# Optimization experiments

Measured on AMD Instinct MI355X. Metric: run time of the kernel, lower is better.

## Reference

```python
import jax, jax.numpy as jnp
import numpy as np

B, N, C = 4, 2304, 256
H = 8                      # num_heads
D = C // H                 # head_dim = 32
SCALE = D ** -0.5
H_DS, W_DS = 48, 48
UP = 2                     # spatial_down_ratio
EPS = 1e-5


def setup_inputs() -> dict:
    key = jax.random.key(0)
    ks = jax.random.split(key, 16)
    g = lambda k, shape, s: (jax.random.normal(k, shape, dtype=jnp.float32) * s)
    return {
        "x1": g(ks[0], (B, N, C), 1.0),
        "x2": g(ks[1], (B, N, C), 1.0),
        # attention projections (torch Linear convention: [out, in], no bias)
        "q1_w": g(ks[2], (C, C), C ** -0.5),
        "kv1_w": g(ks[3], (2 * C, C), C ** -0.5),
        "q2_w": g(ks[4], (C, C), C ** -0.5),
        "kv2_w": g(ks[5], (2 * C, C), C ** -0.5),
        # per-head scalar biases
        "beta12": jnp.full((H,), 0.2, dtype=jnp.float32),
        "beta21": jnp.full((H,), 0.1, dtype=jnp.float32),
        # output projections
        "p1_w": g(ks[6], (C, C), (2.0 / C) ** 0.5),
        "p1_b": g(ks[7], (C,), 1e-2),
        "p2_w": g(ks[8], (C, C), (2.0 / C) ** 0.5),
        "p2_b": g(ks[9], (C,), 1e-2),
        # LayerNorm affine params
        "g1": jnp.ones((C,), dtype=jnp.float32),
        "b1": jnp.zeros((C,), dtype=jnp.float32),
        "g2": jnp.ones((C,), dtype=jnp.float32),
        "b2": jnp.zeros((C,), dtype=jnp.float32),
    }


def _heads(x):
    # [B,N,C] -> [B,H,N,D]
    return x.reshape(B, N, H, D).transpose(0, 2, 1, 3)


def _merge(x):
    # [B,H,N,D] -> [B,N,C]
    return x.transpose(0, 2, 1, 3).reshape(B, N, C)


def _cross_attn(q, k, v, beta):
    # scores: [B,H,N,N] with per-head scalar bias
    s = jnp.einsum("bhqd,bhkd->bhqk", q, k) * SCALE + beta[None, :, None, None]
    a = jax.nn.softmax(s, axis=-1)
    return jnp.einsum("bhqk,bhkd->bhqd", a, v)


def _layernorm(x, g, b):
    mu = jnp.mean(x, axis=-1, keepdims=True)
    var = jnp.var(x, axis=-1, keepdims=True)
    return (x - mu) * jax.lax.rsqrt(var + EPS) * g + b


def _forward(x1, x2, q1_w, kv1_w, q2_w, kv2_w, beta12, beta21,
             p1_w, p1_b, p2_w, p2_b, g1, b1, g2, b2):
    q1 = _heads(x1 @ q1_w.T)
    kv1 = x1 @ kv1_w.T          # [B,N,2C]
    k1, v1 = _heads(kv1[..., :C]), _heads(kv1[..., C:])
    q2 = _heads(x2 @ q2_w.T)
    kv2 = x2 @ kv2_w.T
    k2, v2 = _heads(kv2[..., :C]), _heads(kv2[..., C:])

    o1 = _merge(_cross_attn(q1, k2, v2, beta12))   # x1 attends to x2
    o2 = _merge(_cross_attn(q2, k1, v1, beta21))   # x2 attends to x1

    y1 = _layernorm(jax.nn.relu(o1 @ p1_w.T + p1_b), g1, b1)
    y2 = _layernorm(jax.nn.relu(o2 @ p2_w.T + p2_b), g2, b2)

    # [B,N,C] -> [B,C,H_ds,W_ds]
    y1 = y1.transpose(0, 2, 1).reshape(B, C, H_DS, W_DS)
    y2 = y2.transpose(0, 2, 1).reshape(B, C, H_DS, W_DS)

    # bilinear upsample x2, align_corners=False (half-pixel == jax.image default)
    out_shape = (B, C, H_DS * UP, W_DS * UP)
    y1 = jax.image.resize(y1, out_shape, method="bilinear")
    y2 = jax.image.resize(y2, out_shape, method="bilinear")
    return y1, y2


def reference(x1, x2, q1_w, kv1_w, q2_w, kv2_w, beta12, beta21,
              p1_w, p1_b, p2_w, p2_b, g1, b1, g2, b2):
    return _forward(x1, x2, q1_w, kv1_w, q2_w, kv2_w, beta12, beta21,
                    p1_w, p1_b, p2_w, p2_b, g1, b1, g2, b2)
```

## Files before the change

### kernel.cpp

```cpp
#include <hip/hip_runtime.h>
#include <math.h>


typedef __attribute__((ext_vector_type(8))) short short8;
typedef __attribute__((ext_vector_type(4))) float f32x4;
typedef __attribute__((ext_vector_type(16))) float f32x16;
typedef __attribute__((ext_vector_type(2))) unsigned uint32x2;

#define MFMA16(a, b, c) __builtin_amdgcn_mfma_f32_16x16x32_bf16((a), (b), (c), 0, 0, 0)
#define MFMA32(a, b, c) __builtin_amdgcn_mfma_f32_32x32x16_bf16((a), (b), (c), 0, 0, 0)

__device__ __forceinline__ float bf2f(ushort u) {
    union { unsigned u; float f; } x; x.u = ((unsigned)u) << 16; return x.f;
}
__device__ __forceinline__ ushort f2bf(float f) {
    union { float f; unsigned u; } x; x.f = f;
    unsigned u = x.u;
    return (ushort)((u + 0x7fffu + ((u >> 16) & 1u)) >> 16);
}
__device__ __forceinline__ unsigned cvt_pk_bf16(float a, float b) {
    unsigned r;
    asm("v_cvt_pk_bf16_f32 %0, %1, %2" : "=v"(r) : "v"(a), "v"(b));
    return r;
}
__device__ __forceinline__ float fast_ex2(float x) {
    float r;
    asm("v_exp_f32 %0, %1" : "=v"(r) : "v"(x));
    return r;
}
__device__ __forceinline__ void plswap(unsigned &a, unsigned &b) {
    uint32x2 r = __builtin_amdgcn_permlane32_swap(a, b, false, false);
    a = r[0]; b = r[1];
}

__global__ __launch_bounds__(256) void prep_kernel(
    const void* __restrict__ x1, const void* __restrict__ x2,
    ushort* __restrict__ xo1, ushort* __restrict__ xo2,
    const void* s0, const void* s1, const void* s2, const void* s3,
    const void* s4, const void* s5, const void* s6, const void* s7,
    const void* s8, const void* s9, const void* s10, const void* s11,
    ushort* __restrict__ dst)
{
    ushort u = ((const ushort*)x1)[(threadIdx.x & 63) * 2];
    int e = (u >> 7) & 0xFF;
    int outlier = (e < 100 || e > 135) ? 1 : 0;
    unsigned long long mk = __ballot(outlier);
    int flag = (__popcll(mk) >= 16) ? 1 : 0;

    int bid = blockIdx.x;
    if (bid < 2304) {
        int idx = bid * 256 + threadIdx.x;
        int which = idx >= 294912;
        int off = (which ? idx - 294912 : idx) * 8;
        const void* src = which ? x2 : x1;
        ushort* o = which ? xo2 : xo1;
        if (flag) {
            const float* p = (const float*)src + off;
            float4 a = *(const float4*)p;
            float4 c = *(const float4*)(p + 4);
            uint4 u4;
            u4.x = cvt_pk_bf16(a.x, a.y);
            u4.y = cvt_pk_bf16(a.z, a.w);
            u4.z = cvt_pk_bf16(c.x, c.y);
            u4.w = cvt_pk_bf16(c.z, c.w);
            *(uint4*)(o + off) = u4;
        } else {
            *(uint4*)(o + off) = *(const uint4*)((const ushort*)src + off);
        }
    } else {
        int idx = (bid - 2304) * 256 + threadIdx.x;
        if (idx >= 525824) return;
        const void* src; int off;
        if      (idx < 65536)  { src = s0;  off = idx; }
        else if (idx < 196608) { src = s1;  off = idx - 65536; }
        else if (idx < 262144) { src = s2;  off = idx - 196608; }
        else if (idx < 393216) { src = s3;  off = idx - 262144; }
        else if (idx < 458752) { src = s4;  off = idx - 393216; }
        else if (idx < 524288) { src = s5;  off = idx - 458752; }
        else if (idx < 524544) { src = s6;  off = idx - 524288; }
        else if (idx < 524800) { src = s7;  off = idx - 524544; }
        else if (idx < 525056) { src = s8;  off = idx - 524800; }
        else if (idx < 525312) { src = s9;  off = idx - 525056; }
        else if (idx < 525568) { src = s10; off = idx - 525312; }
        else                   { src = s11; off = idx - 525568; }
        ushort v = flag ? f2bf(((const float*)src)[off])
                        : ((const ushort*)src)[off];
        dst[idx] = v;
    }
}

__global__ __launch_bounds__(256) void gemm_bt(
    const void* __restrict__ Ain, const ushort* __restrict__ W,
    ushort* __restrict__ C, const ushort* __restrict__ bias,
    int M, int N, int K, int relu, const int* __restrict__ dflag, int a_ext,
    int mode, ushort* __restrict__ Kh, ushort* __restrict__ Vt,
    const ushort* __restrict__ W2, const ushort* __restrict__ bias2,
    ushort* __restrict__ Kh2, ushort* __restrict__ Vt2, int mhalf)
{
    __shared__ __align__(16) ushort As[128][40];
    __shared__ __align__(16) ushort Ws[128][40];

    const int m0 = blockIdx.x * 128;
    const int n0 = blockIdx.y * 128;
    const int tid = threadIdx.x;
    const int w = tid >> 6;
    const int wr = w >> 1, wc = w & 1;
    const int lane = tid & 63;
    const int lm = lane & 15;
    const int quad = lane >> 4;
    const int a32 = a_ext ? *dflag : 0;

    const int side = (mhalf && m0 >= mhalf) ? 1 : 0;
    const ushort* Wu = side ? W2 : W;
    const ushort* bu = side ? bias2 : bias;
    ushort* Khu = side ? Kh2 : Kh;
    ushort* Vtu = side ? Vt2 : Vt;

    const f32x4 Z4 = {0.f, 0.f, 0.f, 0.f};
    f32x4 acc[4][4];
    for (int i = 0; i < 4; i++)
        for (int j = 0; j < 4; j++) acc[i][j] = Z4;

    const ushort* A16 = (const ushort*)Ain;
    const float*  A32 = (const float*)Ain;
    const int row = tid >> 1, off16 = (tid & 1) * 16;

    for (int k0 = 0; k0 < K; k0 += 32) {
        __syncthreads();
        if (a32) {
            const float* p0 = A32 + (size_t)(m0 + row) * K + k0 + off16;
            float4 f0 = *(const float4*)p0;
            float4 f1 = *(const float4*)(p0 + 4);
            float4 f2 = *(const float4*)(p0 + 8);
            float4 f3 = *(const float4*)(p0 + 12);
            uint4 t0, t1;
            t0.x = cvt_pk_bf16(f0.x, f0.y);
            t0.y = cvt_pk_bf16(f0.z, f0.w);
            t0.z = cvt_pk_bf16(f1.x, f1.y);
            t0.w = cvt_pk_bf16(f1.z, f1.w);
            t1.x = cvt_pk_bf16(f2.x, f2.y);
            t1.y = cvt_pk_bf16(f2.z, f2.w);
            t1.z = cvt_pk_bf16(f3.x, f3.y);
            t1.w = cvt_pk_bf16(f3.z, f3.w);
            *(uint4*)&As[row][off16]     = t0;
            *(uint4*)&As[row][off16 + 8] = t1;
        } else {
            const ushort* p0 = A16 + (size_t)(m0 + row) * K + k0 + off16;
            *(uint4*)&As[row][off16]     = *(const uint4*)p0;
            *(uint4*)&As[row][off16 + 8] = *(const uint4*)(p0 + 8);
        }
        {
            const ushort* p0 = Wu + (size_t)(n0 + row) * K + k0 + off16;
            *(uint4*)&Ws[row][off16]     = *(const uint4*)p0;
            *(uint4*)&Ws[row][off16 + 8] = *(const uint4*)(p0 + 8);
        }
        __syncthreads();

        short8 af[4], wf[4];
        #pragma unroll
        for (int mt = 0; mt < 4; mt++)
            af[mt] = *(const short8*)&As[wr * 64 + mt * 16 + lm][quad * 8];
        #pragma unroll
        for (int nt = 0; nt < 4; nt++)
            wf[nt] = *(const short8*)&Ws[wc * 64 + nt * 16 + lm][quad * 8];
        #pragma unroll
        for (int mt = 0; mt < 4; mt++)
            #pragma unroll
            for (int nt = 0; nt < 4; nt++)
                acc[mt][nt] = MFMA16(af[mt], wf[nt], acc[mt][nt]);
    }

    if (mode == 1) {
        const float QSC = 0.17677669529663687f * 1.4426950408889634f;
        #pragma unroll
        for (int mt = 0; mt < 4; mt++) {
            const int grow = m0 + wr * 64 + mt * 16 + quad * 4;
            const int grel = grow - (side ? mhalf : 0);
            int bb = grel / 2304;
            int tok = grel - bb * 2304;
            #pragma unroll
            for (int nt = 0; nt < 4; nt++) {
                int col = n0 + wc * 64 + nt * 16 + lm;
                if (col < 256) {
                    for (int r = 0; r < 4; r++)
                        C[(size_t)(grow + r) * 256 + col] = f2bf(acc[mt][nt][r] * QSC);
                } else if (col < 512) {
                    int c2 = col - 256, hh = c2 >> 5, d = c2 & 31;
                    size_t kb = ((size_t)(bb * 8 + hh) * 72 + (tok >> 5)) * 1024
                              + (size_t)(d >> 4) * 512 + (size_t)(d & 15);
                    for (int r = 0; r < 4; r++)
                        Khu[kb + (size_t)((tok + r) & 31) * 16] = f2bf(acc[mt][nt][r]);
                } else {
                    int c2 = col - 512, hh = c2 >> 5, d = c2 & 31;
                    size_t vb = ((size_t)(bb * 8 + hh) * 144 + (tok >> 4)) * 512
                              + (size_t)d * 16 + (size_t)(tok & 15);
                    uint2 o;
                    o.x = cvt_pk_bf16(acc[mt][nt][0], acc[mt][nt][1]);
                    o.y = cvt_pk_bf16(acc[mt][nt][2], acc[mt][nt][3]);
                    *(uint2*)&Vtu[vb] = o;
                }
            }
        }
    } else {
        #pragma unroll
        for (int mt = 0; mt < 4; mt++) {
            const int grow = m0 + wr * 64 + mt * 16 + quad * 4;
            #pragma unroll
            for (int nt = 0; nt < 4; nt++) {
                int col = n0 + wc * 64 + nt * 16 + lm;
                float bv = bu ? bf2f(bu[col]) : 0.f;
                for (int r = 0; r < 4; r++) {
                    float v = acc[mt][nt][r] + bv;
                    if (relu) v = fmaxf(v, 0.f);
                    C[(size_t)(grow + r) * N + col] = f2bf(v);
                }
            }
        }
    }
}

__global__ __launch_bounds__(256) void attn_kernel(
    const ushort* __restrict__ Qa, const ushort* __restrict__ Kha,
    const ushort* __restrict__ Vta, ushort* __restrict__ Oa,
    const ushort* __restrict__ Qb, const ushort* __restrict__ Khb2,
    const ushort* __restrict__ Vtb2, ushort* __restrict__ Ob)
{
    __shared__ unsigned Lo[4][2][64][8];
    __shared__ float    Ll[4][2][64];

    const int sid = blockIdx.x;
    const int qb = blockIdx.y;
    const int side = sid >> 5;
    const int bh = sid & 31;
    const ushort* Q  = side ? Qb   : Qa;
    const ushort* Kh = side ? Khb2 : Kha;
    const ushort* Vt = side ? Vtb2 : Vta;
    ushort* O        = side ? Ob   : Oa;

    const int b = bh >> 3, h = bh & 7;
    const int tid = threadIdx.x;
    const int w = tid >> 6, lane = tid & 63;
    const int l31 = lane & 31, hl = lane >> 5;

    const int qrow0 = qb * 64 + l31;
    const int qrow1 = qrow0 + 32;
    const ushort* qp0 = Q + ((size_t)b * 2304 + qrow0) * 256 + h * 32 + hl * 8;
    const ushort* qp1 = Q + ((size_t)b * 2304 + qrow1) * 256 + h * 32 + hl * 8;
    const short8 qf0a = *(const short8*)qp0;
    const short8 qf1a = *(const short8*)(qp0 + 16);
    const short8 qf0b = *(const short8*)qp1;
    const short8 qf1b = *(const short8*)(qp1 + 16);

    f32x16 oa, ob;
    #pragma unroll
    for (int i = 0; i < 16; i++) { oa[i] = 0.f; ob[i] = 0.f; }
    const f32x16 Z16 = oa;
    float la = 0.f, lb = 0.f;

    const ushort* kp0 = Kh + (size_t)bh * 73728 + l31 * 16 + hl * 8;
    const ushort* vp0 = Vt + (size_t)bh * 73728 + l31 * 16 + hl * 8;

#define LOADT(kf0v, kf1v, vf0v, vf1v, t) { \
    const ushort* _kp = kp0 + (size_t)(t) * 1024; \
    kf0v = *(const short8*)_kp; \
    kf1v = *(const short8*)(_kp + 512); \
    const ushort* _vp = vp0 + (size_t)(t) * 1024; \
    vf0v = *(const short8*)_vp; \
    vf1v = *(const short8*)(_vp + 512); \
}
#define QSET(kf0v, kf1v, vf0v, vf1v, qf0v, qf1v, oacc, lacc) { \
    f32x16 s = MFMA32(kf0v, qf0v, Z16); \
    s = MFMA32(kf1v, qf1v, s); \
    float p[16]; \
    _Pragma("unroll") \
    for (int i = 0; i < 16; i++) p[i] = fast_ex2(s[i]); \
    lacc += (((p[0] + p[1]) + (p[2] + p[3])) + ((p[4] + p[5]) + (p[6] + p[7]))) \
          + (((p[8] + p[9]) + (p[10] + p[11])) + ((p[12] + p[13]) + (p[14] + p[15]))); \
    unsigned c0 = cvt_pk_bf16(p[0],  p[1]); \
    unsigned c1 = cvt_pk_bf16(p[2],  p[3]); \
    unsigned c2 = cvt_pk_bf16(p[4],  p[5]); \
    unsigned c3 = cvt_pk_bf16(p[6],  p[7]); \
    unsigned c4 = cvt_pk_bf16(p[8],  p[9]); \
    unsigned c5 = cvt_pk_bf16(p[10], p[11]); \
    unsigned c6 = cvt_pk_bf16(p[12], p[13]); \
    unsigned c7 = cvt_pk_bf16(p[14], p[15]); \
    plswap(c0, c2); plswap(c1, c3); plswap(c4, c6); plswap(c5, c7); \
    union { unsigned u[4]; short8 s8; } pA, pB; \
    pA.u[0] = c0; pA.u[1] = c1; pA.u[2] = c2; pA.u[3] = c3; \
    pB.u[0] = c4; pB.u[1] = c5; pB.u[2] = c6; pB.u[3] = c7; \
    oacc = MFMA32(vf0v, pA.s8, oacc); \
    oacc = MFMA32(vf1v, pB.s8, oacc); \
}
#define COMP(kf0v, kf1v, vf0v, vf1v) { \
    QSET(kf0v, kf1v, vf0v, vf1v, qf0a, qf1a, oa, la); \
    QSET(kf0v, kf1v, vf0v, vf1v, qf0b, qf1b, ob, lb); \
}

    short8 kA0, kA1, vA0, vA1;
    short8 kB0, kB1, vB0, vB1;

    const int t0 = w * 18;

    LOADT(kA0, kA1, vA0, vA1, t0);
    LOADT(kB0, kB1, vB0, vB1, t0 + 1);

    for (int i = 0; i < 9; i++) {
        COMP(kA0, kA1, vA0, vA1);
        { int ta = t0 + 2 * i + 2; ta = ta < 72 ? ta : 70;
          LOADT(kA0, kA1, vA0, vA1, ta); }
        COMP(kB0, kB1, vB0, vB1);
        { int tb = t0 + 2 * i + 3; tb = tb < 72 ? tb : 71;
          LOADT(kB0, kB1, vB0, vB1, tb); }
    }
#undef LOADT
#undef QSET
#undef COMP

    la += __shfl_xor(la, 32, 64);
    lb += __shfl_xor(lb, 32, 64);

    #pragma unroll
    for (int r = 0; r < 8; r++) {
        Lo[w][0][lane][r] = cvt_pk_bf16(oa[2 * r], oa[2 * r + 1]);
        Lo[w][1][lane][r] = cvt_pk_bf16(ob[2 * r], ob[2 * r + 1]);
    }
    Ll[w][0][lane] = la;
    Ll[w][1][lane] = lb;
    __syncthreads();

    if (w < 2) {
        float os[16];
        #pragma unroll
        for (int r = 0; r < 16; r++) os[r] = 0.f;
        float ls = 0.f;
        #pragma unroll
        for (int u = 0; u < 4; u++) {
            ls += Ll[u][w][lane];
            #pragma unroll
            for (int r = 0; r < 8; r++) {
                unsigned pv = Lo[u][w][lane][r];
                os[2 * r]     += bf2f((ushort)pv);
                os[2 * r + 1] += bf2f((ushort)(pv >> 16));
            }
        }
        float rl = 1.f / ls;
        const int qrow = (w == 0) ? qrow0 : qrow1;
        ushort* op = O + ((size_t)b * 2304 + qrow) * 256 + h * 32 + hl * 4;
        #pragma unroll
        for (int g = 0; g < 4; g++) {
            uint2 o;
            o.x = cvt_pk_bf16(os[4 * g] * rl, os[4 * g + 1] * rl);
            o.y = cvt_pk_bf16(os[4 * g + 2] * rl, os[4 * g + 3] * rl);
            *(uint2*)(op + 8 * g) = o;
        }
    }
}

__global__ __launch_bounds__(256) void projlnt_kernel(
    const ushort* __restrict__ O,
    const ushort* __restrict__ W1c, const ushort* __restrict__ b1v,
    const ushort* __restrict__ g1v, const ushort* __restrict__ t1v,
    const ushort* __restrict__ W2c, const ushort* __restrict__ b2v,
    const ushort* __restrict__ g2v, const ushort* __restrict__ t2v,
    ushort* __restrict__ Yt)
{
    __shared__ __align__(16) ushort As[64][40];
    __shared__ __align__(16) ushort Ws[256][40];
    __shared__ float Sred[4][64][2];

    const int m0 = blockIdx.x * 64;
    const int side = (m0 >= 9216) ? 1 : 0;
    const ushort* Wu = side ? W2c : W1c;
    const ushort* bu = side ? b2v : b1v;
    const ushort* gu = side ? g2v : g1v;
    const ushort* tu = side ? t2v : t1v;

    const int tid = threadIdx.x;
    const int w = tid >> 6, lane = tid & 63;
    const int lm = lane & 15, quad = lane >> 4;

    const f32x4 Z4 = {0.f, 0.f, 0.f, 0.f};
    f32x4 acc[4][4];
    for (int i = 0; i < 4; i++)
        for (int j = 0; j < 4; j++) acc[i][j] = Z4;

    const int arow = tid >> 2, aoff = (tid & 3) * 8;

    for (int k0 = 0; k0 < 256; k0 += 32) {
        __syncthreads();
        *(uint4*)&As[arow][aoff] =
            *(const uint4*)(O + (size_t)(m0 + arow) * 256 + k0 + aoff);
        const ushort* wp = Wu + (size_t)tid * 256 + k0;
        *(uint4*)&Ws[tid][0]  = *(const uint4*)(wp);
        *(uint4*)&Ws[tid][8]  = *(const uint4*)(wp + 8);
        *(uint4*)&Ws[tid][16] = *(const uint4*)(wp + 16);
        *(uint4*)&Ws[tid][24] = *(const uint4*)(wp + 24);
        __syncthreads();

        short8 af[4], wf[4];
        #pragma unroll
        for (int mt = 0; mt < 4; mt++)
            af[mt] = *(const short8*)&As[mt * 16 + lm][quad * 8];
        #pragma unroll
        for (int nt = 0; nt < 4; nt++)
            wf[nt] = *(const short8*)&Ws[w * 64 + nt * 16 + lm][quad * 8];
        #pragma unroll
        for (int mt = 0; mt < 4; mt++)
            #pragma unroll
            for (int nt = 0; nt < 4; nt++)
                acc[mt][nt] = MFMA16(af[mt], wf[nt], acc[mt][nt]);
    }

    #pragma unroll
    for (int nt = 0; nt < 4; nt++) {
        float bv = bf2f(bu[w * 64 + nt * 16 + lm]);
        #pragma unroll
        for (int mt = 0; mt < 4; mt++)
            #pragma unroll
            for (int r = 0; r < 4; r++)
                acc[mt][nt][r] = fmaxf(acc[mt][nt][r] + bv, 0.f);
    }

    float s[4][4], q[4][4];
    #pragma unroll
    for (int mt = 0; mt < 4; mt++)
        #pragma unroll
        for (int r = 0; r < 4; r++) {
            float a0 = acc[mt][0][r], a1 = acc[mt][1][r];
            float a2 = acc[mt][2][r], a3 = acc[mt][3][r];
            s[mt][r] = (a0 + a1) + (a2 + a3);
            q[mt][r] = (a0 * a0 + a1 * a1) + (a2 * a2 + a3 * a3);
        }
    #pragma unroll
    for (int off = 1; off < 16; off <<= 1)
        #pragma unroll
        for (int mt = 0; mt < 4; mt++)
            #pragma unroll
            for (int r = 0; r < 4; r++) {
                s[mt][r] += __shfl_xor(s[mt][r], off, 64);
                q[mt][r] += __shfl_xor(q[mt][r], off, 64);
            }
    if (lm == 0) {
        #pragma unroll
        for (int mt = 0; mt < 4; mt++)
            #pragma unroll
            for (int r = 0; r < 4; r++) {
                int rowl = mt * 16 + quad * 4 + r;
                Sred[w][rowl][0] = s[mt][r];
                Sred[w][rowl][1] = q[mt][r];
            }
    }
    __syncthreads();

    const int mrel = m0 - side * 9216;
    const int bb = mrel / 2304;
    const int tokb = mrel - bb * 2304;
    #pragma unroll
    for (int mt = 0; mt < 4; mt++) {
        float mu[4], rs[4];
        #pragma unroll
        for (int r = 0; r < 4; r++) {
            int rowl = mt * 16 + quad * 4 + r;
            float S = (Sred[0][rowl][0] + Sred[1][rowl][0])
                    + (Sred[2][rowl][0] + Sred[3][rowl][0]);
            float Qq = (Sred[0][rowl][1] + Sred[1][rowl][1])
                     + (Sred[2][rowl][1] + Sred[3][rowl][1]);
            float m = S * (1.f / 256.f);
            float var = Qq * (1.f / 256.f) - m * m;
            mu[r] = m;
            rs[r] = rsqrtf(var + 1e-5f);
        }
        #pragma unroll
        for (int nt = 0; nt < 4; nt++) {
            int col = w * 64 + nt * 16 + lm;
            float g = bf2f(gu[col]);
            float bt = bf2f(tu[col]);
            float y0 = (acc[mt][nt][0] - mu[0]) * rs[0] * g + bt;
            float y1 = (acc[mt][nt][1] - mu[1]) * rs[1] * g + bt;
            float y2 = (acc[mt][nt][2] - mu[2]) * rs[2] * g + bt;
            float y3 = (acc[mt][nt][3] - mu[3]) * rs[3] * g + bt;
            uint2 o;
            o.x = cvt_pk_bf16(y0, y1);
            o.y = cvt_pk_bf16(y2, y3);
            size_t base = ((size_t)((side * 4 + bb) * 256 + col)) * 2304
                        + tokb + mt * 16 + quad * 4;
            *(uint2*)(Yt + base) = o;
        }
    }
}

__global__ __launch_bounds__(256) void upsample_kernel(
    const ushort* __restrict__ Yt, float* __restrict__ out)
{
    int idx = blockIdx.x * 256 + threadIdx.x;
    int t  = idx % 24;
    int r_ = idx / 24;
    int oi = r_ % 96;
    int bc = r_ / 96;

    float fi = oi * 0.5f - 0.25f;
    int i0 = (int)floorf(fi);
    float wi = fi - (float)i0;
    int i1 = i0 + 1 < 47 ? i0 + 1 : 47;
    i0 = i0 > 0 ? i0 : 0;
    int j0 = 2 * t;
    int jm = j0 - 1 > 0 ? j0 - 1 : 0;
    int jp = j0 + 2 < 47 ? j0 + 2 : 47;

    const ushort* r0 = Yt + (size_t)bc * 2304 + i0 * 48;
    const ushort* r1 = Yt + (size_t)bc * 2304 + i1 * 48;
    float a0 = bf2f(r0[jm]), b0 = bf2f(r0[j0]), c0 = bf2f(r0[j0 + 1]), d0 = bf2f(r0[jp]);
    float a1 = bf2f(r1[jm]), b1 = bf2f(r1[j0]), c1 = bf2f(r1[j0 + 1]), d1 = bf2f(r1[jp]);
    float u = 1.f - wi;
    float ha = u * a0 + wi * a1;
    float hb = u * b0 + wi * b1;
    float hc = u * c0 + wi * c1;
    float hd = u * d0 + wi * d1;
    float4 o;
    o.x = 0.25f * ha + 0.75f * hb;
    o.y = 0.75f * hb + 0.25f * hc;
    o.z = 0.25f * hb + 0.75f * hc;
    o.w = 0.75f * hc + 0.25f * hd;
    *(float4*)(out + (size_t)bc * 9216 + oi * 96 + t * 4) = o;
}

extern "C" void kernel_launch(void* const* d_in, const int* in_sizes, int n_in,
                              void* d_out, int out_size, void* d_ws, size_t ws_size,
                              hipStream_t stream)
{
    (void)in_sizes; (void)n_in; (void)out_size; (void)ws_size;

    ushort* ws  = (ushort*)d_ws;
    ushort* Q1  = ws;
    ushort* Q2  = Q1  + 2359296;
    ushort* KV1 = Q2  + 2359296;
    ushort* KV2 = KV1 + 4718592;
    ushort* wc  = KV2 + 4718592;

    ushort* cqkv1w = wc;
    ushort* cqkv2w = wc + 196608;
    ushort* cp1w  = wc + 393216;
    ushort* cp2w  = wc + 458752;
    ushort* cp1b  = wc + 524288;
    ushort* cp2b  = wc + 524544;
    ushort* cg1   = wc + 524800;
    ushort* cb1   = wc + 525056;
    ushort* cg2   = wc + 525312;
    ushort* cb2   = wc + 525568;

    float*  outf = (float*)d_out;
    ushort* O1  = (ushort*)d_out;
    ushort* O2  = O1 + 2359296;
    ushort* Xb1 = O2 + 2359296;
    ushort* Xb2 = Xb1 + 2359296;
    ushort* Yt  = Q1;
    (void)Q2; (void)O2; (void)Xb2;

    dim3 blk(256);
    prep_kernel<<<dim3(4358), blk, 0, stream>>>(
        d_in[0], d_in[1], Xb1, Xb2,
        d_in[2], d_in[3], d_in[4], d_in[5], d_in[8], d_in[10],
        d_in[9], d_in[11], d_in[12], d_in[13], d_in[14], d_in[15],
        wc);

    gemm_bt<<<dim3(144, 6), blk, 0, stream>>>(Xb1, cqkv1w, Q1, nullptr,
        18432, 768, 256, 0, nullptr, 0, 1, KV1, KV1 + 2359296,
        cqkv2w, nullptr, KV2, KV2 + 2359296, 9216);

    attn_kernel<<<dim3(64, 36), blk, 0, stream>>>(
        Q1, KV2, KV2 + 2359296, O1,
        Q2, KV1, KV1 + 2359296, O2);

    projlnt_kernel<<<dim3(288), blk, 0, stream>>>(
        O1, cp1w, cp1b, cg1, cb1, cp2w, cp2b, cg2, cb2, Yt);

    upsample_kernel<<<dim3(18432), blk, 0, stream>>>(Yt, outf);
}
```

Measured before the change: 244.0 us.

## Halve attention query tile per block and spread final reduction across all waves

Each attention block now handles 32 query rows instead of 64, doubling the grid to 64x72 blocks. Each wave runs one QK/PV chain per key tile instead of two. The cross-wave split-K reduction is now shared by all four waves, each writing one 8-column slice, instead of only two waves doing it. This gives more blocks and lower per-thread register pressure, at the cost of loading every K/V tile twice as often from global memory or cache.

Result: slower. 250.6 us (+2.7%).

```diff
diff --git a/kernel.cpp b/kernel.cpp
--- a/kernel.cpp
+++ b/kernel.cpp
@@ -225,8 +225,8 @@
     const ushort* __restrict__ Qb, const ushort* __restrict__ Khb2,
     const ushort* __restrict__ Vtb2, ushort* __restrict__ Ob)
 {
-    __shared__ unsigned Lo[4][2][64][8];
-    __shared__ float    Ll[4][2][64];
+    __shared__ unsigned Lo[4][64][8];
+    __shared__ float    Ll[4][64];
 
     const int sid = blockIdx.x;
     const int qb = blockIdx.y;
@@ -242,20 +242,16 @@
     const int w = tid >> 6, lane = tid & 63;
     const int l31 = lane & 31, hl = lane >> 5;
 
-    const int qrow0 = qb * 64 + l31;
-    const int qrow1 = qrow0 + 32;
+    const int qrow0 = qb * 32 + l31;
     const ushort* qp0 = Q + ((size_t)b * 2304 + qrow0) * 256 + h * 32 + hl * 8;
-    const ushort* qp1 = Q + ((size_t)b * 2304 + qrow1) * 256 + h * 32 + hl * 8;
     const short8 qf0a = *(const short8*)qp0;
     const short8 qf1a = *(const short8*)(qp0 + 16);
-    const short8 qf0b = *(const short8*)qp1;
-    const short8 qf1b = *(const short8*)(qp1 + 16);
-
-    f32x16 oa, ob;
-    #pragma unroll
-    for (int i = 0; i < 16; i++) { oa[i] = 0.f; ob[i] = 0.f; }
+
+    f32x16 oa;
+    #pragma unroll
+    for (int i = 0; i < 16; i++) oa[i] = 0.f;
     const f32x16 Z16 = oa;
-    float la = 0.f, lb = 0.f;
+    float la = 0.f;
 
     const ushort* kp0 = Kh + (size_t)bh * 73728 + l31 * 16 + hl * 8;
     const ushort* vp0 = Vt + (size_t)bh * 73728 + l31 * 16 + hl * 8;
@@ -268,14 +264,14 @@
     vf0v = *(const short8*)_vp; \
     vf1v = *(const short8*)(_vp + 512); \
 }
-#define QSET(kf0v, kf1v, vf0v, vf1v, qf0v, qf1v, oacc, lacc) { \
-    f32x16 s = MFMA32(kf0v, qf0v, Z16); \
-    s = MFMA32(kf1v, qf1v, s); \
+#define QSET(kf0v, kf1v, vf0v, vf1v) { \
+    f32x16 s = MFMA32(kf0v, qf0a, Z16); \
+    s = MFMA32(kf1v, qf1a, s); \
     float p[16]; \
     _Pragma("unroll") \
     for (int i = 0; i < 16; i++) p[i] = fast_ex2(s[i]); \
-    lacc += (((p[0] + p[1]) + (p[2] + p[3])) + ((p[4] + p[5]) + (p[6] + p[7]))) \
-          + (((p[8] + p[9]) + (p[10] + p[11])) + ((p[12] + p[13]) + (p[14] + p[15]))); \
+    la += (((p[0] + p[1]) + (p[2] + p[3])) + ((p[4] + p[5]) + (p[6] + p[7]))) \
+        + (((p[8] + p[9]) + (p[10] + p[11])) + ((p[12] + p[13]) + (p[14] + p[15]))); \
     unsigned c0 = cvt_pk_bf16(p[0],  p[1]); \
     unsigned c1 = cvt_pk_bf16(p[2],  p[3]); \
     unsigned c2 = cvt_pk_bf16(p[4],  p[5]); \
@@ -288,12 +284,8 @@
     union { unsigned u[4]; short8 s8; } pA, pB; \
     pA.u[0] = c0; pA.u[1] = c1; pA.u[2] = c2; pA.u[3] = c3; \
     pB.u[0] = c4; pB.u[1] = c5; pB.u[2] = c6; pB.u[3] = c7; \
-    oacc = MFMA32(vf0v, pA.s8, oacc); \
-    oacc = MFMA32(vf1v, pB.s8, oacc); \
-}
-#define COMP(kf0v, kf1v, vf0v, vf1v) { \
-    QSET(kf0v, kf1v, vf0v, vf1v, qf0a, qf1a, oa, la); \
-    QSET(kf0v, kf1v, vf0v, vf1v, qf0b, qf1b, ob, lb); \
+    oa = MFMA32(vf0v, pA.s8, oa); \
+    oa = MFMA32(vf1v, pB.s8, oa); \
 }
 
     short8 kA0, kA1, vA0, vA1;
@@ -305,55 +297,41 @@
     LOADT(kB0, kB1, vB0, vB1, t0 + 1);
 
     for (int i = 0; i < 9; i++) {
-        COMP(kA0, kA1, vA0, vA1);
+        QSET(kA0, kA1, vA0, vA1);
         { int ta = t0 + 2 * i + 2; ta = ta < 72 ? ta : 70;
           LOADT(kA0, kA1, vA0, vA1, ta); }
-        COMP(kB0, kB1, vB0, vB1);
+        QSET(kB0, kB1, vB0, vB1);
         { int tb = t0 + 2 * i + 3; tb = tb < 72 ? tb : 71;
           LOADT(kB0, kB1, vB0, vB1, tb); }
     }
 #undef LOADT
 #undef QSET
-#undef COMP
 
     la += __shfl_xor(la, 32, 64);
-    lb += __shfl_xor(lb, 32, 64);
-
-    #pragma unroll
-    for (int r = 0; r < 8; r++) {
-        Lo[w][0][lane][r] = cvt_pk_bf16(oa[2 * r], oa[2 * r + 1]);
-        Lo[w][1][lane][r] = cvt_pk_bf16(ob[2 * r], ob[2 * r + 1]);
-    }
-    Ll[w][0][lane] = la;
-    Ll[w][1][lane] = lb;
+
+    #pragma unroll
+    for (int r = 0; r < 8; r++)
+        Lo[w][lane][r] = cvt_pk_bf16(oa[2 * r], oa[2 * r + 1]);
+    Ll[w][lane] = la;
     __syncthreads();
 
-    if (w < 2) {
-        float os[16];
-        #pragma unroll
-        for (int r = 0; r < 16; r++) os[r] = 0.f;
-        float ls = 0.f;
-        #pragma unroll
-        for (int u = 0; u < 4; u++) {
-            ls += Ll[u][w][lane];
-            #pragma unroll
-            for (int r = 0; r < 8; r++) {
-                unsigned pv = Lo[u][w][lane][r];
-                os[2 * r]     += bf2f((ushort)pv);
-                os[2 * r + 1] += bf2f((ushort)(pv >> 16));
-            }
-        }
-        float rl = 1.f / ls;
-        const int qrow = (w == 0) ? qrow0 : qrow1;
-        ushort* op = O + ((size_t)b * 2304 + qrow) * 256 + h * 32 + hl * 4;
-        #pragma unroll
-        for (int g = 0; g < 4; g++) {
-            uint2 o;
-            o.x = cvt_pk_bf16(os[4 * g] * rl, os[4 * g + 1] * rl);
-            o.y = cvt_pk_bf16(os[4 * g + 2] * rl, os[4 * g + 3] * rl);
-            *(uint2*)(op + 8 * g) = o;
-        }
-    }
+    float ls = (Ll[0][lane] + Ll[1][lane]) + (Ll[2][lane] + Ll[3][lane]);
+    float os0 = 0.f, os1 = 0.f, os2 = 0.f, os3 = 0.f;
+    #pragma unroll
+    for (int u = 0; u < 4; u++) {
+        unsigned p0 = Lo[u][lane][2 * w];
+        unsigned p1 = Lo[u][lane][2 * w + 1];
+        os0 += bf2f((ushort)p0);
+        os1 += bf2f((ushort)(p0 >> 16));
+        os2 += bf2f((ushort)p1);
+        os3 += bf2f((ushort)(p1 >> 16));
+    }
+    float rl = 1.f / ls;
+    ushort* op = O + ((size_t)b * 2304 + qrow0) * 256 + h * 32 + hl * 4;
+    uint2 o;
+    o.x = cvt_pk_bf16(os0 * rl, os1 * rl);
+    o.y = cvt_pk_bf16(os2 * rl, os3 * rl);
+    *(uint2*)(op + 8 * w) = o;
 }
 
 __global__ __launch_bounds__(256) void projlnt_kernel(
@@ -567,7 +545,7 @@
         18432, 768, 256, 0, nullptr, 0, 1, KV1, KV1 + 2359296,
         cqkv2w, nullptr, KV2, KV2 + 2359296, 9216);
 
-    attn_kernel<<<dim3(64, 36), blk, 0, stream>>>(
+    attn_kernel<<<dim3(64, 72), blk, 0, stream>>>(
         Q1, KV2, KV2 + 2359296, O1,
         Q2, KV1, KV1 + 2359296, O2);
 
```

## Compute softmax exp2 with packed fp16 polynomial and fp16 PV MFMA

Applied to the files above, without the earlier changes.

Replaces the per-element v_exp_f32 transcendental in the attention inner loop with a packed-fp16 exp2 approximation: a range clamp, a magic-number split into integer and fraction parts, a cubic polynomial, and exponent insertion by shift-add, two values per instruction. P and V are now kept in fp16, so the V projection epilogue writes fp16 and the PV product uses the f16 MFMA instead of bf16. The aim is to relieve the transcendental-unit and VALU bottleneck of the softmax. In exchange, row sums are partly accumulated in fp16 and V is stored in fp16, which lowers accuracy and risks overflow or precision loss.

Result: slower. 280.4 us (+14.9%).

```diff
diff --git a/kernel.cpp b/kernel.cpp
--- a/kernel.cpp
+++ b/kernel.cpp
@@ -3,12 +3,14 @@
 
 
 typedef __attribute__((ext_vector_type(8))) short short8;
+typedef __attribute__((ext_vector_type(8))) _Float16 half8;
 typedef __attribute__((ext_vector_type(4))) float f32x4;
 typedef __attribute__((ext_vector_type(16))) float f32x16;
 typedef __attribute__((ext_vector_type(2))) unsigned uint32x2;
 
 #define MFMA16(a, b, c) __builtin_amdgcn_mfma_f32_16x16x32_bf16((a), (b), (c), 0, 0, 0)
 #define MFMA32(a, b, c) __builtin_amdgcn_mfma_f32_32x32x16_bf16((a), (b), (c), 0, 0, 0)
+#define MFMA32H(a, b, c) __builtin_amdgcn_mfma_f32_32x32x16_f16((a), (b), (c), 0, 0, 0)
 
 __device__ __forceinline__ float bf2f(ushort u) {
     union { unsigned u; float f; } x; x.u = ((unsigned)u) << 16; return x.f;
@@ -23,10 +25,28 @@
     asm("v_cvt_pk_bf16_f32 %0, %1, %2" : "=v"(r) : "v"(a), "v"(b));
     return r;
 }
-__device__ __forceinline__ float fast_ex2(float x) {
-    float r;
-    asm("v_exp_f32 %0, %1" : "=v"(r) : "v"(x));
+__device__ __forceinline__ unsigned pk_cvt_f16(float a, float b) {
+    unsigned r;
+    asm("v_cvt_pkrtz_f16_f32 %0, %1, %2" : "=v"(r) : "v"(a), "v"(b));
     return r;
+}
+__device__ __forceinline__ unsigned pk_addf(unsigned a, unsigned b) {
+    unsigned r; asm("v_pk_add_f16 %0, %1, %2" : "=v"(r) : "v"(a), "v"(b)); return r;
+}
+__device__ __forceinline__ unsigned pk_maxf(unsigned a, unsigned b) {
+    unsigned r; asm("v_pk_max_f16 %0, %1, %2" : "=v"(r) : "v"(a), "v"(b)); return r;
+}
+__device__ __forceinline__ unsigned pk_fmaf(unsigned a, unsigned b, unsigned c) {
+    unsigned r; asm("v_pk_fma_f16 %0, %1, %2, %3" : "=v"(r) : "v"(a), "v"(b), "v"(c)); return r;
+}
+__device__ __forceinline__ unsigned pk_lshl(unsigned sh, unsigned a) {
+    unsigned r; asm("v_pk_lshlrev_b16 %0, %1, %2" : "=v"(r) : "v"(sh), "v"(a)); return r;
+}
+__device__ __forceinline__ unsigned pk_addu(unsigned a, unsigned b) {
+    unsigned r; asm("v_pk_add_u16 %0, %1, %2" : "=v"(r) : "v"(a), "v"(b)); return r;
+}
+__device__ __forceinline__ float cvt_f32_lo(unsigned h) {
+    float r; asm("v_cvt_f32_f16 %0, %1" : "=v"(r) : "v"(h)); return r;
 }
 __device__ __forceinline__ void plswap(unsigned &a, unsigned &b) {
     uint32x2 r = __builtin_amdgcn_permlane32_swap(a, b, false, false);
@@ -195,8 +215,8 @@
                     size_t vb = ((size_t)(bb * 8 + hh) * 144 + (tok >> 4)) * 512
                               + (size_t)d * 16 + (size_t)(tok & 15);
                     uint2 o;
-                    o.x = cvt_pk_bf16(acc[mt][nt][0], acc[mt][nt][1]);
-                    o.y = cvt_pk_bf16(acc[mt][nt][2], acc[mt][nt][3]);
+                    o.x = pk_cvt_f16(acc[mt][nt][0], acc[mt][nt][1]);
+                    o.y = pk_cvt_f16(acc[mt][nt][2], acc[mt][nt][3]);
                     *(uint2*)&Vtu[vb] = o;
                 }
             }
@@ -251,6 +271,16 @@
     const short8 qf0b = *(const short8*)qp1;
     const short8 qf1b = *(const short8*)(qp1 + 16);
 
+    const unsigned MN13   = 0xCA80CA80u;
+    const unsigned M1536  = 0x66006600u;
+    const unsigned MN1536 = 0xE600E600u;
+    const unsigned MNEG1  = 0xBC00BC00u;
+    const unsigned C3     = 0x2B1A2B1Au;
+    const unsigned C2     = 0x33B033B0u;
+    const unsigned C1     = 0x398C398Cu;
+    const unsigned C0     = 0x3C003C00u;
+    const unsigned SH10   = 0x000A000Au;
+
     f32x16 oa, ob;
     #pragma unroll
     for (int i = 0; i < 16; i++) { oa[i] = 0.f; ob[i] = 0.f; }
@@ -271,25 +301,38 @@
 #define QSET(kf0v, kf1v, vf0v, vf1v, qf0v, qf1v, oacc, lacc) { \
     f32x16 s = MFMA32(kf0v, qf0v, Z16); \
     s = MFMA32(kf1v, qf1v, s); \
-    float p[16]; \
+    unsigned P0, P1, P2, P3, P4, P5, P6, P7; \
     _Pragma("unroll") \
-    for (int i = 0; i < 16; i++) p[i] = fast_ex2(s[i]); \
-    lacc += (((p[0] + p[1]) + (p[2] + p[3])) + ((p[4] + p[5]) + (p[6] + p[7]))) \
-          + (((p[8] + p[9]) + (p[10] + p[11])) + ((p[12] + p[13]) + (p[14] + p[15]))); \
-    unsigned c0 = cvt_pk_bf16(p[0],  p[1]); \
-    unsigned c1 = cvt_pk_bf16(p[2],  p[3]); \
-    unsigned c2 = cvt_pk_bf16(p[4],  p[5]); \
-    unsigned c3 = cvt_pk_bf16(p[6],  p[7]); \
-    unsigned c4 = cvt_pk_bf16(p[8],  p[9]); \
-    unsigned c5 = cvt_pk_bf16(p[10], p[11]); \
-    unsigned c6 = cvt_pk_bf16(p[12], p[13]); \
-    unsigned c7 = cvt_pk_bf16(p[14], p[15]); \
-    plswap(c0, c2); plswap(c1, c3); plswap(c4, c6); plswap(c5, c7); \
-    union { unsigned u[4]; short8 s8; } pA, pB; \
-    pA.u[0] = c0; pA.u[1] = c1; pA.u[2] = c2; pA.u[3] = c3; \
-    pB.u[0] = c4; pB.u[1] = c5; pB.u[2] = c6; pB.u[3] = c7; \
-    oacc = MFMA32(vf0v, pA.s8, oacc); \
-    oacc = MFMA32(vf1v, pB.s8, oacc); \
+    for (int i = 0; i < 8; i++) { \
+        unsigned z = pk_cvt_f16(s[2 * i], s[2 * i + 1]); \
+        z = pk_maxf(z, MN13); \
+        unsigned T = pk_addf(z, M1536); \
+        unsigned nf = pk_addf(T, MN1536); \
+        unsigned f = pk_fmaf(nf, MNEG1, z); \
+        unsigned py = pk_fmaf(f, C3, C2); \
+        py = pk_fmaf(f, py, C1); \
+        py = pk_fmaf(f, py, C0); \
+        unsigned pb = pk_addu(py, pk_lshl(SH10, T)); \
+        switch (i) { \
+            case 0: P0 = pb; break; case 1: P1 = pb; break; \
+            case 2: P2 = pb; break; case 3: P3 = pb; break; \
+            case 4: P4 = pb; break; case 5: P5 = pb; break; \
+            case 6: P6 = pb; break; default: P7 = pb; break; } \
+    } \
+    { \
+        unsigned t01 = pk_addf(P0, P1), t23 = pk_addf(P2, P3); \
+        unsigned t45 = pk_addf(P4, P5), t67 = pk_addf(P6, P7); \
+        unsigned tt = pk_addf(pk_addf(t01, t23), pk_addf(t45, t67)); \
+        lacc += cvt_f32_lo(tt) + cvt_f32_lo(tt >> 16); \
+    } \
+    plswap(P0, P2); plswap(P1, P3); plswap(P4, P6); plswap(P5, P7); \
+    union { unsigned u[4]; half8 h8; } pA, pB, vA_, vB_; \
+    pA.u[0] = P0; pA.u[1] = P1; pA.u[2] = P2; pA.u[3] = P3; \
+    pB.u[0] = P4; pB.u[1] = P5; pB.u[2] = P6; pB.u[3] = P7; \
+    union { short8 s8; half8 h8; } vc0, vc1; \
+    vc0.s8 = vf0v; vc1.s8 = vf1v; \
+    oacc = MFMA32H(vc0.h8, pA.h8, oacc); \
+    oacc = MFMA32H(vc1.h8, pB.h8, oacc); \
 }
 #define COMP(kf0v, kf1v, vf0v, vf1v) { \
     QSET(kf0v, kf1v, vf0v, vf1v, qf0a, qf1a, oa, la); \
```
